# Optimization experiments

Measured on AMD Instinct MI355X. Metric: run time of the kernel, lower is better.

Reference implementation:

```python
import jax, jax.numpy as jnp
import numpy as np


def _flip_roll(a):
    # torch.roll(torch.flip(a, [-3,-2,-1]), (1,1,1), [-3,-2,-1])
    return jnp.roll(jnp.flip(a, axis=(-3, -2, -1)), shift=(1, 1, 1), axis=(-3, -2, -1))


def dht_3d(x):
    dims = (2, 3, 4)
    r = jnp.fft.fftn(x, axes=dims).real - jnp.fft.fftn(jnp.flip(x, axis=-1), axes=dims).imag
    norm = jnp.sqrt(jnp.sum(r * r, axis=dims, keepdims=True))
    safe = jnp.where(norm == 0, 1.0, norm)
    return jnp.where(norm != 0, r / safe, jnp.zeros_like(r))


def compl_mul3d(x1, x2):
    x1n = _flip_roll(x1)
    x2n = _flip_roll(x2)
    return 0.5 * (
        jnp.einsum('bixyz,ioxyz->boxyz', x1, x2)
        - jnp.einsum('bixyz,ioxyz->boxyz', x1n, x2n)
        + jnp.einsum('bixyz,ioxyz->boxyz', x1, x2n)
        + jnp.einsum('bixyz,ioxyz->boxyz', x1n, x2)
    )


def idht_3d(X):
    n = X.shape[2] * X.shape[3] * X.shape[4]
    return dht_3d(X) / n


def setup_inputs() -> dict:
    key = jax.random.key(0)
    k1, k2 = jax.random.split(key)
    B, Cin, Cout = 4, 32, 32
    S = 64
    M = 8
    scale = 1.0 / (Cin * Cout)
    x = jax.random.normal(k1, (B, Cin, S, S, S), dtype=jnp.float32)
    weights1 = scale * jax.random.uniform(k2, (Cin, Cout, M, M, M), dtype=jnp.float32)
    return {"x": x, "weights1": weights1}


def reference(x, weights1):
    B = x.shape[0]
    Cout = weights1.shape[1]
    m1, m2, m3 = weights1.shape[2], weights1.shape[3], weights1.shape[4]
    s1, s2, s3 = x.shape[-3], x.shape[-2], x.shape[-1]
    x_ht = dht_3d(x)
    conv = compl_mul3d(x_ht[:, :, :m1, :m2, :m3], weights1)
    out_ht = jnp.zeros((B, Cout, s1, s2, s3), dtype=x.dtype)
    out_ht = out_ht.at[:, :, :m1, :m2, :m3].set(conv)
    return idht_3d(out_ht)
```

## Files before the change

### kernel.cpp

```cpp
#include <hip/hip_runtime.h>
#include <math.h>


constexpr int NT = 262144;
constexpr float TWOPI_64 = 0.09817477042468103f;


__global__ __launch_bounds__(256) void k_fwd1(const float* __restrict__ x,
                                              float* __restrict__ S,
                                              float* __restrict__ red1p) {
  __shared__ float As[64 * 68];
  __shared__ float Bs[64 * 68];
  __shared__ float PL[32 * 65];
  __shared__ float c64v[64], s64v[64];
  __shared__ float rsm[12];
  const int t = threadIdx.x;
  const int j = blockIdx.x;
  const int bc = blockIdx.y;
  const int n1a = j, n1b = (64 - j) & 63;
  const bool paired = (n1a != n1b);
  if (t < 64) { float ang = TWOPI_64 * t; c64v[t] = cosf(ang); s64v[t] = sinf(ang); }
  const float4* xa4 = (const float4*)(x + ((size_t)bc << 18) + (n1a << 12));
  const float4* xb4 = (const float4*)(x + ((size_t)bc << 18) + (n1b << 12));
  float ssp = 0.f;
  for (int q = 0; q < 4; ++q) {
    int l4 = t + (q << 8);
    int fl = l4 << 2;
    int r = fl >> 6, c = fl & 63;
    float4 va = xa4[l4], vb = xb4[l4];
    *(float4*)&As[r * 68 + c] = va;
    *(float4*)&Bs[r * 68 + c] = vb;
    ssp += va.x * va.x + va.y * va.y + va.z * va.z + va.w * va.w;
    if (paired) ssp += vb.x * vb.x + vb.y * vb.y + vb.z * vb.z + vb.w * vb.w;
  }
  __syncthreads();
  const int n2 = t & 63;
  const int k3a = t >> 6, k3b = k3a + 4;
  {
    float ca = 1.f, sa = 0.f, cb = 1.f, sb = 0.f;
    const float dca = c64v[k3a], dsa = s64v[k3a];
    const float dcb = c64v[k3b], dsb = s64v[k3b];
    float reA0 = 0, imA0 = 0, reA1 = 0, imA1 = 0;
    float reB0 = 0, imB0 = 0, reB1 = 0, imB1 = 0;
    const float4* Ar = (const float4*)&As[n2 * 68];
    const float4* Br = (const float4*)&Bs[n2 * 68];
    for (int m = 0; m < 16; ++m) {
      float4 va = Ar[m], vb = Br[m];
      float av[4] = {va.x, va.y, va.z, va.w};
      float bv[4] = {vb.x, vb.y, vb.z, vb.w};
#pragma unroll
      for (int e = 0; e < 4; ++e) {
        float a = av[e], b = bv[e];
        reA0 += a * ca; imA0 -= a * sa;
        reB0 += b * ca; imB0 -= b * sa;
        reA1 += a * cb; imA1 -= a * sb;
        reB1 += b * cb; imB1 -= b * sb;
        float nca = ca * dca - sa * dsa; sa = sa * dca + ca * dsa; ca = nca;
        float ncb = cb * dcb - sb * dsb; sb = sb * dcb + cb * dsb; cb = ncb;
      }
    }
    PL[(k3a) * 65 + n2] = reA0;      PL[(8 + k3a) * 65 + n2] = imA0;
    PL[(16 + k3a) * 65 + n2] = reB0; PL[(24 + k3a) * 65 + n2] = imB0;
    PL[(k3b) * 65 + n2] = reA1;      PL[(8 + k3b) * 65 + n2] = imA1;
    PL[(16 + k3b) * 65 + n2] = reB1; PL[(24 + k3b) * 65 + n2] = imB1;
  }
  float c1p = 0.f, c2p = 0.f;
  for (int q = 0; q < 16; ++q) {
    int l = t + (q << 8);
    int r = l >> 6, c = l & 63;
    float a = As[r * 68 + c];
    int m2 = (64 - r) & 63;
    int m3 = (64 - c) & 63;
    int m3b = (62 - c) & 63;
    c1p += a * Bs[m2 * 68 + m3];
    c2p += a * Bs[m2 * 68 + m3b];
  }
  if (paired) { c1p *= 2.f; c2p *= 2.f; }
  for (int off = 32; off; off >>= 1) {
    ssp += __shfl_down(ssp, off);
    c1p += __shfl_down(c1p, off);
    c2p += __shfl_down(c2p, off);
  }
  const int lane = t & 63, wid = t >> 6;
  if (lane == 0) { rsm[wid * 3] = ssp; rsm[wid * 3 + 1] = c1p; rsm[wid * 3 + 2] = c2p; }
  __syncthreads();
  if (t == 0) {
    red1p[((size_t)bc * 33 + j) * 3 + 0] = rsm[0] + rsm[3] + rsm[6] + rsm[9];
    red1p[((size_t)bc * 33 + j) * 3 + 1] = rsm[1] + rsm[4] + rsm[7] + rsm[10];
    red1p[((size_t)bc * 33 + j) * 3 + 2] = rsm[2] + rsm[5] + rsm[8] + rsm[11];
  }
  {
    const int k2 = t & 7;
    const int rr = t >> 3;
    const int row = rr >> 4, f = (rr >> 3) & 1, k3 = rr & 7;
    float rc = 1.f, rs = 0.f;
    const float dc = c64v[k2], ds = s64v[k2];
    float re = 0.f, im = 0.f;
    const float* pr = &PL[rr * 65];
    for (int n2i = 0; n2i < 64; ++n2i) {
      float v = pr[n2i];
      re += v * rc; im -= v * rs;
      float nc = rc * dc - rs * ds; rs = rs * dc + rc * ds; rc = nc;
    }
    const int n1row = row ? n1b : n1a;
    ((float2*)S)[(((size_t)bc * 64 + n1row) * 2 + f) * 64 + k2 * 8 + k3] =
        make_float2(re, im);
  }
}

__global__ __launch_bounds__(256) void k_fwd2s(const float* __restrict__ S,
                                               const float* __restrict__ red1p,
                                               float* __restrict__ xh) {
  __shared__ float2 U3L[512];
  __shared__ float c64v[64], s64v[64];
  __shared__ float rbuf[99];
  const int t = threadIdx.x;
  const int h = blockIdx.x;
  const int bc = blockIdx.y;
  if (t < 64) { float ang = TWOPI_64 * t; c64v[t] = cosf(ang); s64v[t] = sinf(ang); }
  if (t < 99) rbuf[t] = red1p[(size_t)bc * 99 + t];
  __syncthreads();
  {
    const int kkl = t & 31;
    const int f = (t >> 5) & 1;
    const int k1g = t >> 6;
    const int rr2 = f * 64 + h * 32 + kkl;
    const float2* Sb = (const float2*)(S + ((size_t)bc << 14));
    float rc[2], rs[2], dc[2], ds[2], re[2], im[2];
#pragma unroll
    for (int m = 0; m < 2; ++m) {
      int k1 = k1g * 2 + m;
      rc[m] = 1.f; rs[m] = 0.f; dc[m] = c64v[k1]; ds[m] = s64v[k1];
      re[m] = 0.f; im[m] = 0.f;
    }
#pragma unroll 4
    for (int n1 = 0; n1 < 64; ++n1) {
      float2 ab = Sb[(n1 << 7) + rr2];
#pragma unroll
      for (int m = 0; m < 2; ++m) {
        re[m] += ab.x * rc[m] + ab.y * rs[m];
        im[m] += ab.y * rc[m] - ab.x * rs[m];
        float nc = rc[m] * dc[m] - rs[m] * ds[m];
        rs[m] = rs[m] * dc[m] + rc[m] * ds[m];
        rc[m] = nc;
      }
    }
#pragma unroll
    for (int m = 0; m < 2; ++m) {
      int k1 = k1g * 2 + m;
      U3L[f * 256 + k1 * 32 + kkl] = make_float2(re[m], im[m]);
    }
  }
  __syncthreads();
  float ss = 0.f, c1 = 0.f, c2 = 0.f;
  for (int jj = 0; jj < 33; ++jj) {
    ss += rbuf[jj * 3];
    c1 += rbuf[jj * 3 + 1];
    c2 += rbuf[jj * 3 + 2];
  }
  float nsq = 0.5f * (float)NT * (2.f * ss + c1 - c2);
  float inv1 = nsq > 0.f ? rsqrtf(nsq) : 0.f;
  {
    const int k1 = t >> 5, kkl = t & 31;
    const int kk = h * 32 + kkl;
    const int k3 = kk & 7;
    float2 U = U3L[k1 * 32 + kkl];
    float2 V = U3L[256 + k1 * 32 + kkl];
    float ct = c64v[k3], st = s64v[k3];
    float r = U.x - V.y - st * (U.x + V.y) - ct * (U.y - V.x);
    xh[(size_t)bc * 512 + k1 * 64 + kk] = r * inv1;
  }
}

__global__ __launch_bounds__(256) void k_mixA(const float* __restrict__ xh,
                                              const float* __restrict__ w,
                                              float* __restrict__ A1,
                                              float* __restrict__ inv2) {
  __shared__ float xsh[16384];
  const int t = threadIdx.x;
  const int bc2 = blockIdx.x;
  const int b = bc2 >> 5, o = bc2 & 31;
  const float4* xb4 = (const float4*)(xh + ((size_t)b << 14));
  float4* xs4 = (float4*)xsh;
  for (int q = 0; q < 16; ++q) xs4[t + (q << 8)] = xb4[t + (q << 8)];
  __syncthreads();
  float acc0 = 0.f, acc1 = 0.f;
  {
    int k0 = t, kq1 = t + 256;
    int k1 = k0 >> 6, k2 = (k0 >> 3) & 7, k3 = k0 & 7;
    int nk0 = (((8 - k1) & 7) << 6) + (((8 - k2) & 7) << 3) + ((8 - k3) & 7);
    int l1 = kq1 >> 6, l2 = (kq1 >> 3) & 7, l3 = kq1 & 7;
    int nk1 = (((8 - l1) & 7) << 6) + (((8 - l2) & 7) << 3) + ((8 - l3) & 7);
    for (int i = 0; i < 32; ++i) {
      const float* wr = w + (((size_t)i * 32 + o) << 9);
      float xa0 = xsh[(i << 9) + k0],  xn0 = xsh[(i << 9) + nk0];
      float xa1 = xsh[(i << 9) + kq1], xn1 = xsh[(i << 9) + nk1];
      acc0 += (xa0 + xn0) * wr[k0]  + (xa0 - xn0) * wr[nk0];
      acc1 += (xa1 + xn1) * wr[kq1] + (xa1 - xn1) * wr[nk1];
    }
  }
  __syncthreads();
  xsh[t] = 0.5f * acc0;
  xsh[t + 256] = 0.5f * acc1;
  if (t < 64) {
    float ang = TWOPI_64 * t;
    xsh[512 + t] = cosf(ang);
    xsh[576 + t] = sinf(ang);
  }
  __syncthreads();
  const int col = t & 63;
  const int quarter = t >> 6;
  float cv[8];
#pragma unroll
  for (int n1 = 0; n1 < 8; ++n1) cv[n1] = xsh[(n1 << 6) + col];
  if (quarter == 0) {
    float p = 0.f;
#pragma unroll
    for (int n1 = 0; n1 < 8; ++n1) p += cv[n1] * cv[n1];
    for (int off = 32; off; off >>= 1) p += __shfl_down(p, off);
    if (t == 0) {
      float c000 = cv[0];
      float nsq = 0.5f * (float)NT * (2.f * p + c000 * c000);
      float nrm = sqrtf(nsq);
      inv2[bc2] = nrm > 0.f ? 1.f / (nrm * (float)NT) : 0.f;
    }
  }
  float2* A1p = (float2*)(A1 + ((size_t)bc2 << 13));
  for (int it = 0; it < 16; ++it) {
    int k1 = quarter + (it << 2);
    float re = 0.f, im = 0.f;
#pragma unroll
    for (int n1 = 0; n1 < 8; ++n1) {
      int a = (k1 * n1) & 63;
      re += cv[n1] * xsh[512 + a];
      im -= cv[n1] * xsh[576 + a];
    }
    A1p[(k1 << 6) + col] = make_float2(re, im);
  }
}

__global__ __launch_bounds__(256) void k_expBC(const float* __restrict__ A1,
                                               const float* __restrict__ inv2,
                                               float* __restrict__ out) {
  __shared__ float arow[128];
  __shared__ float B2[64 * 20];
  __shared__ float c64v[64], s64v[64];
  const int t = threadIdx.x;
  const int k1 = blockIdx.x;
  const int bc2 = blockIdx.y;
  if (t < 64) { float ang = TWOPI_64 * t; c64v[t] = cosf(ang); s64v[t] = sinf(ang); }
  if (t < 128) arow[t] = A1[((size_t)bc2 << 13) + (k1 << 7) + t];
  __syncthreads();
  {
    const int k2 = t & 63;
    const int g = t >> 6;
    const int f = g & 1;
    const int n3h = (g >> 1) << 2;
    float acc[4] = {0, 0, 0, 0};
    for (int n2i = 0; n2i < 8; ++n2i) {
      int a_ = (k2 * n2i) & 63;
      float tc = c64v[a_], ts = s64v[a_];
      const float4* ar4 = (const float4*)&arow[((n2i << 3) + n3h) << 1];
      float4 p0 = ar4[0];
      float4 p1 = ar4[1];
      if (f == 0) {
        acc[0] += p0.x * tc + p0.y * ts;
        acc[1] += p0.z * tc + p0.w * ts;
        acc[2] += p1.x * tc + p1.y * ts;
        acc[3] += p1.z * tc + p1.w * ts;
      } else {
        acc[0] += p0.y * tc - p0.x * ts;
        acc[1] += p0.w * tc - p0.z * ts;
        acc[2] += p1.y * tc - p1.x * ts;
        acc[3] += p1.w * tc - p1.z * ts;
      }
    }
    *(float4*)&B2[k2 * 20 + (f << 3) + n3h] = make_float4(acc[0], acc[1], acc[2], acc[3]);
  }
  __syncthreads();
  {
    const int k3 = t & 63;
    const int wid = t >> 6;
    float C1r[8], C2r[8];
#pragma unroll
    for (int n3 = 0; n3 < 8; ++n3) {
      int a0 = (k3 * n3) & 63;
      int a1 = (k3 * (n3 + 1)) & 63;
      C1r[n3] = c64v[a0] - s64v[a1];
      C2r[n3] = s64v[a0] - c64v[a1];
    }
    const float sc = inv2[bc2];
    float* dst = out + ((size_t)bc2 << 18) + (k1 << 12);
    for (int it = 0; it < 16; ++it) {
      int k2 = (wid << 4) + it;
      const float4* br4 = (const float4*)&B2[k2 * 20];
      float4 r0 = br4[0], r1 = br4[1], r2 = br4[2], r3 = br4[3];
      float acc = r0.x * C1r[0] + r0.y * C1r[1] + r0.z * C1r[2] + r0.w * C1r[3]
                + r1.x * C1r[4] + r1.y * C1r[5] + r1.z * C1r[6] + r1.w * C1r[7]
                + r2.x * C2r[0] + r2.y * C2r[1] + r2.z * C2r[2] + r2.w * C2r[3]
                + r3.x * C2r[4] + r3.y * C2r[5] + r3.z * C2r[6] + r3.w * C2r[7];
      dst[(k2 << 6) + k3] = acc * sc;
    }
  }
}

extern "C" void kernel_launch(void* const* d_in, const int* in_sizes, int n_in,
                              void* d_out, int out_size, void* d_ws, size_t ws_size,
                              hipStream_t stream) {
  const float* x = (const float*)d_in[0];
  const float* w = (const float*)d_in[1];
  float* out = (float*)d_out;
  float* ws = (float*)d_ws;
  float* S     = ws;
  float* red1p = ws + 2097152;
  float* xh    = ws + 2109824;
  float* inv2  = ws + 2175360;
  float* A1    = ws + 2175488;

  k_fwd1 <<<dim3(33, 128), 256, 0, stream>>>(x, S, red1p);
  k_fwd2s<<<dim3(2, 128),  256, 0, stream>>>(S, red1p, xh);
  k_mixA <<<dim3(128),     256, 0, stream>>>(xh, w, A1, inv2);
  k_expBC<<<dim3(64, 128), 256, 0, stream>>>(A1, inv2, out);
}
```

Before: 275.3 us.

## Use shared-memory twiddle tables and split fwd2s/mixA blocks for more parallelism

Replaces the recursive rotation-based twiddle updates in k_fwd1 and k_fwd2s with precomputed shared-memory cos/sin tables, which shortens dependency chains and should improve accuracy. k_fwd2s now launches 4 blocks per channel instead of 2, and k_mixA 256 blocks instead of 128, each doing half the columns. Because mixA's norm is now split across two blocks, it writes two partial sums that k_expBC combines into the scale factor. In exchange the table setup adds shared memory, extra sin/cos work per block and more LDS loads.

Result: no change. 271.3 us (-1.5%).

```diff
diff --git a/kernel.cpp b/kernel.cpp
--- a/kernel.cpp
+++ b/kernel.cpp
@@ -12,14 +12,19 @@
   __shared__ float As[64 * 68];
   __shared__ float Bs[64 * 68];
   __shared__ float PL[32 * 65];
-  __shared__ float c64v[64], s64v[64];
+  __shared__ float tw1[1024];
   __shared__ float rsm[12];
   const int t = threadIdx.x;
   const int j = blockIdx.x;
   const int bc = blockIdx.y;
   const int n1a = j, n1b = (64 - j) & 63;
   const bool paired = (n1a != n1b);
-  if (t < 64) { float ang = TWOPI_64 * t; c64v[t] = cosf(ang); s64v[t] = sinf(ang); }
+  for (int u = t; u < 1024; u += 256) {
+    int n3 = u >> 4, k3q = (u >> 2) & 3, jj = u & 3;
+    int k3 = k3q + ((jj >> 1) << 2);
+    float ang = TWOPI_64 * (float)((k3 * n3) & 63);
+    tw1[u] = (jj & 1) ? sinf(ang) : cosf(ang);
+  }
   const float4* xa4 = (const float4*)(x + ((size_t)bc << 18) + (n1a << 12));
   const float4* xb4 = (const float4*)(x + ((size_t)bc << 18) + (n1b << 12));
   float ssp = 0.f;
@@ -35,34 +40,31 @@
   }
   __syncthreads();
   const int n2 = t & 63;
-  const int k3a = t >> 6, k3b = k3a + 4;
-  {
-    float ca = 1.f, sa = 0.f, cb = 1.f, sb = 0.f;
-    const float dca = c64v[k3a], dsa = s64v[k3a];
-    const float dcb = c64v[k3b], dsb = s64v[k3b];
+  const int k3q = t >> 6;
+  {
     float reA0 = 0, imA0 = 0, reA1 = 0, imA1 = 0;
     float reB0 = 0, imB0 = 0, reB1 = 0, imB1 = 0;
     const float4* Ar = (const float4*)&As[n2 * 68];
     const float4* Br = (const float4*)&Bs[n2 * 68];
+    const float4* T4 = (const float4*)tw1;
     for (int m = 0; m < 16; ++m) {
       float4 va = Ar[m], vb = Br[m];
       float av[4] = {va.x, va.y, va.z, va.w};
       float bv[4] = {vb.x, vb.y, vb.z, vb.w};
 #pragma unroll
       for (int e = 0; e < 4; ++e) {
+        float4 tw = T4[(m << 4) + (e << 2) + k3q];
         float a = av[e], b = bv[e];
-        reA0 += a * ca; imA0 -= a * sa;
-        reB0 += b * ca; imB0 -= b * sa;
-        reA1 += a * cb; imA1 -= a * sb;
-        reB1 += b * cb; imB1 -= b * sb;
-        float nca = ca * dca - sa * dsa; sa = sa * dca + ca * dsa; ca = nca;
-        float ncb = cb * dcb - sb * dsb; sb = sb * dcb + cb * dsb; cb = ncb;
+        reA0 += a * tw.x; imA0 -= a * tw.y;
+        reB0 += b * tw.x; imB0 -= b * tw.y;
+        reA1 += a * tw.z; imA1 -= a * tw.w;
+        reB1 += b * tw.z; imB1 -= b * tw.w;
       }
     }
-    PL[(k3a) * 65 + n2] = reA0;      PL[(8 + k3a) * 65 + n2] = imA0;
-    PL[(16 + k3a) * 65 + n2] = reB0; PL[(24 + k3a) * 65 + n2] = imB0;
-    PL[(k3b) * 65 + n2] = reA1;      PL[(8 + k3b) * 65 + n2] = imA1;
-    PL[(16 + k3b) * 65 + n2] = reB1; PL[(24 + k3b) * 65 + n2] = imB1;
+    PL[(k3q) * 65 + n2] = reA0;       PL[(8 + k3q) * 65 + n2] = imA0;
+    PL[(16 + k3q) * 65 + n2] = reB0;  PL[(24 + k3q) * 65 + n2] = imB0;
+    PL[(4 + k3q) * 65 + n2] = reA1;   PL[(12 + k3q) * 65 + n2] = imA1;
+    PL[(20 + k3q) * 65 + n2] = reB1;  PL[(28 + k3q) * 65 + n2] = imB1;
   }
   float c1p = 0.f, c2p = 0.f;
   for (int q = 0; q < 16; ++q) {
@@ -93,14 +95,14 @@
     const int k2 = t & 7;
     const int rr = t >> 3;
     const int row = rr >> 4, f = (rr >> 3) & 1, k3 = rr & 7;
-    float rc = 1.f, rs = 0.f;
-    const float dc = c64v[k2], ds = s64v[k2];
     float re = 0.f, im = 0.f;
     const float* pr = &PL[rr * 65];
+    const int tb = ((k2 & 3) << 2) + ((k2 >> 2) << 1);
+#pragma unroll 4
     for (int n2i = 0; n2i < 64; ++n2i) {
       float v = pr[n2i];
-      re += v * rc; im -= v * rs;
-      float nc = rc * dc - rs * ds; rs = rs * dc + rc * ds; rc = nc;
+      const float2 cs = *(const float2*)&tw1[(n2i << 4) + tb];
+      re += v * cs.x; im -= v * cs.y;
     }
     const int n1row = row ? n1b : n1a;
     ((float2*)S)[(((size_t)bc * 64 + n1row) * 2 + f) * 64 + k2 * 8 + k3] =
@@ -111,45 +113,35 @@
 __global__ __launch_bounds__(256) void k_fwd2s(const float* __restrict__ S,
                                                const float* __restrict__ red1p,
                                                float* __restrict__ xh) {
-  __shared__ float2 U3L[512];
-  __shared__ float c64v[64], s64v[64];
+  __shared__ float2 U3L[256];
+  __shared__ float2 tw[8 * 66];
   __shared__ float rbuf[99];
   const int t = threadIdx.x;
   const int h = blockIdx.x;
   const int bc = blockIdx.y;
-  if (t < 64) { float ang = TWOPI_64 * t; c64v[t] = cosf(ang); s64v[t] = sinf(ang); }
+  for (int u = t; u < 512; u += 256) {
+    int k1 = u >> 6, n1 = u & 63;
+    float ang = TWOPI_64 * (float)((k1 * n1) & 63);
+    tw[k1 * 66 + n1] = make_float2(cosf(ang), sinf(ang));
+  }
   if (t < 99) rbuf[t] = red1p[(size_t)bc * 99 + t];
   __syncthreads();
   {
-    const int kkl = t & 31;
-    const int f = (t >> 5) & 1;
-    const int k1g = t >> 6;
-    const int rr2 = f * 64 + h * 32 + kkl;
+    const int kkl = t & 15;
+    const int f = (t >> 4) & 1;
+    const int k1 = t >> 5;
+    const int rr2 = f * 64 + h * 16 + kkl;
     const float2* Sb = (const float2*)(S + ((size_t)bc << 14));
-    float rc[2], rs[2], dc[2], ds[2], re[2], im[2];
-#pragma unroll
-    for (int m = 0; m < 2; ++m) {
-      int k1 = k1g * 2 + m;
-      rc[m] = 1.f; rs[m] = 0.f; dc[m] = c64v[k1]; ds[m] = s64v[k1];
-      re[m] = 0.f; im[m] = 0.f;
-    }
+    const float2* tk = &tw[k1 * 66];
+    float re = 0.f, im = 0.f;
 #pragma unroll 4
     for (int n1 = 0; n1 < 64; ++n1) {
       float2 ab = Sb[(n1 << 7) + rr2];
-#pragma unroll
-      for (int m = 0; m < 2; ++m) {
-        re[m] += ab.x * rc[m] + ab.y * rs[m];
-        im[m] += ab.y * rc[m] - ab.x * rs[m];
-        float nc = rc[m] * dc[m] - rs[m] * ds[m];
-        rs[m] = rs[m] * dc[m] + rc[m] * ds[m];
-        rc[m] = nc;
-      }
-    }
-#pragma unroll
-    for (int m = 0; m < 2; ++m) {
-      int k1 = k1g * 2 + m;
-      U3L[f * 256 + k1 * 32 + kkl] = make_float2(re[m], im[m]);
-    }
+      float2 cs = tk[n1];
+      re += ab.x * cs.x + ab.y * cs.y;
+      im += ab.y * cs.x - ab.x * cs.y;
+    }
+    U3L[f * 128 + k1 * 16 + kkl] = make_float2(re, im);
   }
   __syncthreads();
   float ss = 0.f, c1 = 0.f, c2 = 0.f;
@@ -160,14 +152,14 @@
   }
   float nsq = 0.5f * (float)NT * (2.f * ss + c1 - c2);
   float inv1 = nsq > 0.f ? rsqrtf(nsq) : 0.f;
-  {
-    const int k1 = t >> 5, kkl = t & 31;
-    const int kk = h * 32 + kkl;
+  if (t < 128) {
+    const int k1 = t >> 4, kkl = t & 15;
+    const int kk = h * 16 + kkl;
     const int k3 = kk & 7;
-    float2 U = U3L[k1 * 32 + kkl];
-    float2 V = U3L[256 + k1 * 32 + kkl];
-    float ct = c64v[k3], st = s64v[k3];
-    float r = U.x - V.y - st * (U.x + V.y) - ct * (U.y - V.x);
+    float2 U = U3L[k1 * 16 + kkl];
+    float2 V = U3L[128 + k1 * 16 + kkl];
+    float2 cs = tw[k3 * 66 + 1];
+    float r = U.x - V.y - cs.y * (U.x + V.y) - cs.x * (U.y - V.x);
     xh[(size_t)bc * 512 + k1 * 64 + kk] = r * inv1;
   }
 }
@@ -175,72 +167,66 @@
 __global__ __launch_bounds__(256) void k_mixA(const float* __restrict__ xh,
                                               const float* __restrict__ w,
                                               float* __restrict__ A1,
-                                              float* __restrict__ inv2) {
+                                              float* __restrict__ inv2q) {
   __shared__ float xsh[16384];
+  __shared__ float convL[8 * 33];
+  __shared__ float c64v[64], s64v[64];
+  __shared__ float psum[4];
   const int t = threadIdx.x;
-  const int bc2 = blockIdx.x;
+  const int bh = blockIdx.x;
+  const int h = bh & 1;
+  const int bc2 = bh >> 1;
   const int b = bc2 >> 5, o = bc2 & 31;
+  if (t < 64) { float ang = TWOPI_64 * t; c64v[t] = cosf(ang); s64v[t] = sinf(ang); }
   const float4* xb4 = (const float4*)(xh + ((size_t)b << 14));
   float4* xs4 = (float4*)xsh;
   for (int q = 0; q < 16; ++q) xs4[t + (q << 8)] = xb4[t + (q << 8)];
   __syncthreads();
-  float acc0 = 0.f, acc1 = 0.f;
-  {
-    int k0 = t, kq1 = t + 256;
-    int k1 = k0 >> 6, k2 = (k0 >> 3) & 7, k3 = k0 & 7;
-    int nk0 = (((8 - k1) & 7) << 6) + (((8 - k2) & 7) << 3) + ((8 - k3) & 7);
-    int l1 = kq1 >> 6, l2 = (kq1 >> 3) & 7, l3 = kq1 & 7;
-    int nk1 = (((8 - l1) & 7) << 6) + (((8 - l2) & 7) << 3) + ((8 - l3) & 7);
-    for (int i = 0; i < 32; ++i) {
-      const float* wr = w + (((size_t)i * 32 + o) << 9);
-      float xa0 = xsh[(i << 9) + k0],  xn0 = xsh[(i << 9) + nk0];
-      float xa1 = xsh[(i << 9) + kq1], xn1 = xsh[(i << 9) + nk1];
-      acc0 += (xa0 + xn0) * wr[k0]  + (xa0 - xn0) * wr[nk0];
-      acc1 += (xa1 + xn1) * wr[kq1] + (xa1 - xn1) * wr[nk1];
-    }
-  }
-  __syncthreads();
-  xsh[t] = 0.5f * acc0;
-  xsh[t + 256] = 0.5f * acc1;
-  if (t < 64) {
-    float ang = TWOPI_64 * t;
-    xsh[512 + t] = cosf(ang);
-    xsh[576 + t] = sinf(ang);
-  }
-  __syncthreads();
-  const int col = t & 63;
-  const int quarter = t >> 6;
+  const int n1m = t >> 5;
+  const int col32 = t & 31;
+  const int col = (h << 5) + col32;
+  const int n2 = col >> 3, n3 = col & 7;
+  const int k = (n1m << 6) + col;
+  const int nk = (((8 - n1m) & 7) << 6) + (((8 - n2) & 7) << 3) + ((8 - n3) & 7);
+  float acc = 0.f;
+  const float* wb = w + ((size_t)o << 9);
+#pragma unroll 4
+  for (int i = 0; i < 32; ++i) {
+    const float* wr = wb + ((size_t)i << 14);
+    float xa = xsh[(i << 9) + k], xn = xsh[(i << 9) + nk];
+    acc += (xa + xn) * wr[k] + (xa - xn) * wr[nk];
+  }
+  const float cval = 0.5f * acc;
+  convL[n1m * 33 + col32] = cval;
+  float p = cval * cval;
+  for (int off = 32; off; off >>= 1) p += __shfl_down(p, off);
+  if ((t & 63) == 0) psum[t >> 6] = p;
+  __syncthreads();
+  if (t == 0) {
+    float Q = 2.f * (psum[0] + psum[1] + psum[2] + psum[3]);
+    if (h == 0) { float c000 = convL[0]; Q += c000 * c000; }
+    inv2q[bc2 * 2 + h] = Q;
+  }
+  const int q8 = t >> 5;
   float cv[8];
 #pragma unroll
-  for (int n1 = 0; n1 < 8; ++n1) cv[n1] = xsh[(n1 << 6) + col];
-  if (quarter == 0) {
-    float p = 0.f;
-#pragma unroll
-    for (int n1 = 0; n1 < 8; ++n1) p += cv[n1] * cv[n1];
-    for (int off = 32; off; off >>= 1) p += __shfl_down(p, off);
-    if (t == 0) {
-      float c000 = cv[0];
-      float nsq = 0.5f * (float)NT * (2.f * p + c000 * c000);
-      float nrm = sqrtf(nsq);
-      inv2[bc2] = nrm > 0.f ? 1.f / (nrm * (float)NT) : 0.f;
-    }
-  }
+  for (int n1i = 0; n1i < 8; ++n1i) cv[n1i] = convL[n1i * 33 + col32];
   float2* A1p = (float2*)(A1 + ((size_t)bc2 << 13));
-  for (int it = 0; it < 16; ++it) {
-    int k1 = quarter + (it << 2);
+  for (int it = 0; it < 8; ++it) {
+    const int k1 = q8 + (it << 3);
     float re = 0.f, im = 0.f;
 #pragma unroll
-    for (int n1 = 0; n1 < 8; ++n1) {
-      int a = (k1 * n1) & 63;
-      re += cv[n1] * xsh[512 + a];
-      im -= cv[n1] * xsh[576 + a];
+    for (int n1i = 0; n1i < 8; ++n1i) {
+      int a = (k1 * n1i) & 63;
+      re += cv[n1i] * c64v[a];
+      im -= cv[n1i] * s64v[a];
     }
     A1p[(k1 << 6) + col] = make_float2(re, im);
   }
 }
 
 __global__ __launch_bounds__(256) void k_expBC(const float* __restrict__ A1,
-                                               const float* __restrict__ inv2,
+                                               const float* __restrict__ inv2q,
                                                float* __restrict__ out) {
   __shared__ float arow[128];
   __shared__ float B2[64 * 20];
@@ -248,6 +234,7 @@
   const int t = threadIdx.x;
   const int k1 = blockIdx.x;
   const int bc2 = blockIdx.y;
+  const float q0 = inv2q[bc2 * 2], q1 = inv2q[bc2 * 2 + 1];
   if (t < 64) { float ang = TWOPI_64 * t; c64v[t] = cosf(ang); s64v[t] = sinf(ang); }
   if (t < 128) arow[t] = A1[((size_t)bc2 << 13) + (k1 << 7) + t];
   __syncthreads();
@@ -289,7 +276,8 @@
       C1r[n3] = c64v[a0] - s64v[a1];
       C2r[n3] = s64v[a0] - c64v[a1];
     }
-    const float sc = inv2[bc2];
+    float nsq = 0.5f * (float)NT * (q0 + q1);
+    const float sc = nsq > 0.f ? 1.f / (sqrtf(nsq) * (float)NT) : 0.f;
     float* dst = out + ((size_t)bc2 << 18) + (k1 << 12);
     for (int it = 0; it < 16; ++it) {
       int k2 = (wid << 4) + it;
@@ -314,11 +302,11 @@
   float* S     = ws;
   float* red1p = ws + 2097152;
   float* xh    = ws + 2109824;
-  float* inv2  = ws + 2175360;
-  float* A1    = ws + 2175488;
+  float* inv2q = ws + 2175360;
+  float* A1    = ws + 2175616;
 
   k_fwd1 <<<dim3(33, 128), 256, 0, stream>>>(x, S, red1p);
-  k_fwd2s<<<dim3(2, 128),  256, 0, stream>>>(S, red1p, xh);
-  k_mixA <<<dim3(128),     256, 0, stream>>>(xh, w, A1, inv2);
-  k_expBC<<<dim3(64, 128), 256, 0, stream>>>(A1, inv2, out);
-}
+  k_fwd2s<<<dim3(4, 128),  256, 0, stream>>>(S, red1p, xh);
+  k_mixA <<<dim3(256),     256, 0, stream>>>(xh, w, A1, inv2q);
+  k_expBC<<<dim3(64, 128), 256, 0, stream>>>(A1, inv2q, out);
+}
```
